# Optimization experiments

Measured on AMD Instinct MI355X. Metric: run time of the kernel, lower is better.

The kernel has to match this reference:

```python
import jax, jax.numpy as jnp
import numpy as np

N = 50000      # nodes
E = 800000     # edges (avg degree 16)
D_IN = 128
D_H = 128
D_OUT = 8


def setup_inputs() -> dict:
    key = jax.random.key(0)
    ks = jax.random.split(key, 12)
    def lin(k, fan_in, shape):
        return (jax.random.normal(k, shape, jnp.float32) / np.float32(np.sqrt(fan_in)))
    return {
        "node_features": jax.random.normal(ks[0], (N, D_IN), jnp.float32),
        "edge_index": jax.random.randint(ks[1], (2, E), 0, N, jnp.int32),
        # 3 GCNConv layers: weight [in, out] + bias [out]
        "W0": lin(ks[2], D_IN, (D_IN, D_H)), "b0": jnp.zeros((D_H,), jnp.float32),
        "W1": lin(ks[3], D_H, (D_H, D_H)),  "b1": jnp.zeros((D_H,), jnp.float32),
        "W2": lin(ks[4], D_H, (D_H, D_H)),  "b2": jnp.zeros((D_H,), jnp.float32),
        # classifier MLP: hidden -> hidden//2 -> output
        "cW1": lin(ks[5], D_H, (D_H, D_H // 2)), "cb1": jnp.zeros((D_H // 2,), jnp.float32),
        "cW2": lin(ks[6], D_H // 2, (D_H // 2, D_OUT)), "cb2": jnp.zeros((D_OUT,), jnp.float32),
    }


def _gcn_norm(edge_index, n):
    # PyG GCNConv default: add self-loops, symmetric D^-1/2 (A+I) D^-1/2 normalization
    loops = jnp.arange(n, dtype=edge_index.dtype)
    src = jnp.concatenate([edge_index[0], loops])   # message sources j
    dst = jnp.concatenate([edge_index[1], loops])   # aggregation targets i
    deg = jax.ops.segment_sum(jnp.ones_like(src, dtype=jnp.float32), dst, num_segments=n)
    dinv = jax.lax.rsqrt(jnp.maximum(deg, 1.0))     # deg >= 1 due to self-loops
    norm = dinv[src] * dinv[dst]                    # [E+N]
    return src, dst, norm


def _gcn_conv(x, W, b, src, dst, norm, n):
    h = x @ W                                        # [N, out] dense transform first (PyG order)
    msg = h[src] * norm[:, None]                     # gather + scale  [E+N, out]
    out = jax.ops.segment_sum(msg, dst, num_segments=n)  # scatter-add
    return out + b


def reference(node_features, edge_index, W0, b0, W1, b1, W2, b2, cW1, cb1, cW2, cb2):
    n = node_features.shape[0]
    src, dst, norm = _gcn_norm(edge_index, n)
    x = jax.nn.relu(_gcn_conv(node_features, W0, b0, src, dst, norm, n))  # dropout is identity in eval
    x = jax.nn.relu(_gcn_conv(x, W1, b1, src, dst, norm, n))
    x = _gcn_conv(x, W2, b2, src, dst, norm, n)       # last conv: no relu/dropout
    # classifier MLP (dropout identity in eval)
    h = jax.nn.relu(x @ cW1 + cb1)
    return h @ cW2 + cb2                              # [N, D_OUT]
```

## Files before the change

### kernel.cpp

```cpp
#include <hip/hip_runtime.h>
#include <hip/hip_fp16.h>


#define CAP 48
#define FPG 256

using half8v  = __attribute__((ext_vector_type(8))) _Float16;
using float4v = __attribute__((ext_vector_type(4))) float;

__global__ __launch_bounds__(256) void fill_kernel(const int* __restrict__ src,
                                                   const int* __restrict__ dst, int e, int n,
                                                   const float* __restrict__ W0,
                                                   const float* __restrict__ W1,
                                                   const float* __restrict__ W2,
                                                   const float* __restrict__ cW1,
                                                   const float* __restrict__ cb1,
                                                   const float* __restrict__ b2,
                                                   int* __restrict__ cnt,
                                                   unsigned short* __restrict__ col,
                                                   __half* __restrict__ Wf0,
                                                   __half* __restrict__ Wf1,
                                                   __half* __restrict__ Wfc,
                                                   float* __restrict__ bc) {
    int b = blockIdx.x;
    int tid = threadIdx.x;
    const int FILLB = 8 * FPG;
    if (b < FILLB) {
        int g = b & 7;
        int cb = b >> 3;
        int npp = (n + 7) >> 3;
        int lo = g * npp;
        int hi = min(lo + npp, n);
        int step = FPG * 256;
        int base = cb * 256 + tid;
        int dv[13], sv[13];
        #pragma unroll
        for (int k = 0; k < 13; k++) {
            int i = base + k * step;
            if (i < e) {
                dv[k] = __builtin_nontemporal_load(dst + i);
                sv[k] = __builtin_nontemporal_load(src + i);
            }
        }
        #pragma unroll
        for (int k = 0; k < 13; k++) {
            int i = base + k * step;
            if (i < e) {
                int d = dv[k];
                if (d >= lo && d < hi) {
                    int c = atomicAdd(&cnt[d], 1);
                    if (c < CAP) col[d * CAP + c] = (unsigned short)sv[k];
                }
            }
        }
        return;
    }
    b -= FILLB;
    if (b < 16) {
        int t = b * 256 + tid;
        const float* W = (t < 2048) ? W0 : W1;
        __half* Wf = (t < 2048) ? Wf0 : Wf1;
        int u = t & 2047;
        int lane = u & 63, tile = (u >> 6) & 7, kk = u >> 9;
        int k0 = kk * 32 + (lane >> 4) * 8;
        int nn = tile * 16 + (lane & 15);
        __half tmp[8];
        #pragma unroll
        for (int j = 0; j < 8; j++) tmp[j] = __float2half(W[(k0 + j) * 128 + nn]);
        *(float4*)(Wf + (size_t)u * 8) = *(const float4*)tmp;
        return;
    }
    b -= 16;
    if (b < 4) {
        int u = b * 256 + tid;
        int lane = u & 63, tile = (u >> 6) & 3, kk = u >> 8;
        int k0 = kk * 32 + (lane >> 4) * 8;
        int nn = tile * 16 + (lane & 15);
        float a[8] = {};
        for (int m = 0; m < 128; m++) {
            float c = cW1[m * 64 + nn];
            #pragma unroll
            for (int j = 0; j < 8; j++) a[j] = fmaf(W2[(k0 + j) * 128 + m], c, a[j]);
        }
        __half tmp[8];
        #pragma unroll
        for (int j = 0; j < 8; j++) tmp[j] = __float2half(a[j]);
        *(float4*)(Wfc + (size_t)u * 8) = *(const float4*)tmp;
        return;
    }
    if (tid < 64) {
        float a = cb1[tid];
        for (int k = 0; k < 128; k++) a = fmaf(b2[k], cW1[k * 64 + tid], a);
        bc[tid] = a;
    }
}

__global__ __launch_bounds__(256) void gemm0_mfma(const float* __restrict__ x,
                                                  const __half* __restrict__ Wf,
                                                  const int* __restrict__ cnt,
                                                  __half* __restrict__ out, int n) {
    int tid = threadIdx.x;
    int wv = tid >> 6, lane = tid & 63;
    int row0 = blockIdx.x * 64 + wv * 16;
    int m = lane & 15, q = lane >> 4;
    int ra = min(row0 + m, n - 1);
    const float* xrow = x + (size_t)ra * 128 + q * 8;
    const _Float16* wf = (const _Float16*)Wf + (size_t)lane * 8;
    float4v acc[8] = {};
    #pragma unroll
    for (int kk = 0; kk < 4; kk++) {
        float4 xa = *(const float4*)(xrow + kk * 32);
        float4 xb = *(const float4*)(xrow + kk * 32 + 4);
        half8v a;
        a[0] = (_Float16)xa.x; a[1] = (_Float16)xa.y;
        a[2] = (_Float16)xa.z; a[3] = (_Float16)xa.w;
        a[4] = (_Float16)xb.x; a[5] = (_Float16)xb.y;
        a[6] = (_Float16)xb.z; a[7] = (_Float16)xb.w;
        #pragma unroll
        for (int t8 = 0; t8 < 8; t8++) {
            half8v bfr = *(const half8v*)(wf + (size_t)(kk * 8 + t8) * 512);
            acc[t8] = __builtin_amdgcn_mfma_f32_16x16x32_f16(a, bfr, acc[t8], 0, 0, 0);
        }
    }
    int rowv[4];
    float dr[4];
    #pragma unroll
    for (int r = 0; r < 4; r++) {
        rowv[r] = row0 + q * 4 + r;
        dr[r] = (rowv[r] < n) ? rsqrtf((float)(cnt[rowv[r]] + 1)) : 0.f;
    }
    #pragma unroll
    for (int t8 = 0; t8 < 8; t8++) {
        #pragma unroll
        for (int r = 0; r < 4; r++) {
            if (rowv[r] < n)
                out[(size_t)(t8 >> 1) * n * 32 + (size_t)rowv[r] * 32 + (t8 & 1) * 16 + m] =
                    __float2half(acc[t8][r] * dr[r]);
        }
    }
}

__global__ __launch_bounds__(256) void gemm_mfma(const __half* __restrict__ x,
                                                 const __half* __restrict__ Wf,
                                                 const int* __restrict__ cnt,
                                                 __half* __restrict__ out, int n) {
    int tid = threadIdx.x;
    int wv = tid >> 6, lane = tid & 63;
    int row0 = blockIdx.x * 64 + wv * 16;
    int m = lane & 15, q = lane >> 4;
    int ra = min(row0 + m, n - 1);
    const _Float16* xb = (const _Float16*)x;
    const _Float16* wf = (const _Float16*)Wf + (size_t)lane * 8;
    float4v acc[8] = {};
    #pragma unroll
    for (int kk = 0; kk < 4; kk++) {
        int tki = kk * 2 + (q >> 1);
        half8v a = *(const half8v*)(xb + (size_t)(tki >> 1) * n * 32 + (size_t)ra * 32 +
                                    (tki & 1) * 16 + (q & 1) * 8);
        #pragma unroll
        for (int t8 = 0; t8 < 8; t8++) {
            half8v bfr = *(const half8v*)(wf + (size_t)(kk * 8 + t8) * 512);
            acc[t8] = __builtin_amdgcn_mfma_f32_16x16x32_f16(a, bfr, acc[t8], 0, 0, 0);
        }
    }
    int rowv[4];
    float dr[4];
    #pragma unroll
    for (int r = 0; r < 4; r++) {
        rowv[r] = row0 + q * 4 + r;
        dr[r] = (rowv[r] < n) ? rsqrtf((float)(cnt[rowv[r]] + 1)) : 0.f;
    }
    #pragma unroll
    for (int t8 = 0; t8 < 8; t8++) {
        #pragma unroll
        for (int r = 0; r < 4; r++) {
            if (rowv[r] < n)
                out[(size_t)(t8 >> 1) * n * 32 + (size_t)rowv[r] * 32 + (t8 & 1) * 16 + m] =
                    __float2half(acc[t8][r] * dr[r]);
        }
    }
}

__global__ __launch_bounds__(256) void agg_tiled(const __half* __restrict__ hin,
                                                 const int* __restrict__ cnt,
                                                 const unsigned short* __restrict__ col,
                                                 const float* __restrict__ bias,
                                                 __half* __restrict__ hout,
                                                 int n, int relu, int scale_out) {
    int ft = blockIdx.x & 3;
    int nb = blockIdx.x >> 2;
    int tid = threadIdx.x;
    int node = nb * 64 + (tid >> 2);
    int q = tid & 3;
    int ic = min(node, n - 1);
    const _Float16* hsl = (const _Float16*)hin + (size_t)ft * n * 32 + q * 8;
    int ci = cnt[ic];
    int len = min(ci, CAP);
    float di = rsqrtf((float)(ci + 1));
    half8v s = *(const half8v*)(hsl + (size_t)ic * 32);
    float acc[8];
    #pragma unroll
    for (int t = 0; t < 8; t++) acc[t] = (float)s[t];
    const unsigned short* crow = col + ic * CAP;
    int nfull = len >> 4;
    for (int f = 0; f < nfull; f++) {
        int k0 = f * 16;
        uint4 ca = *(const uint4*)(crow + k0);
        uint4 cb = *(const uint4*)(crow + k0 + 8);
        int j[16];
        j[0]  = ca.x & 0xffff; j[1]  = ca.x >> 16;
        j[2]  = ca.y & 0xffff; j[3]  = ca.y >> 16;
        j[4]  = ca.z & 0xffff; j[5]  = ca.z >> 16;
        j[6]  = ca.w & 0xffff; j[7]  = ca.w >> 16;
        j[8]  = cb.x & 0xffff; j[9]  = cb.x >> 16;
        j[10] = cb.y & 0xffff; j[11] = cb.y >> 16;
        j[12] = cb.z & 0xffff; j[13] = cb.z >> 16;
        j[14] = cb.w & 0xffff; j[15] = cb.w >> 16;
        half8v v[16];
        #pragma unroll
        for (int u = 0; u < 16; u++) v[u] = *(const half8v*)(hsl + (size_t)j[u] * 32);
        #pragma unroll
        for (int u = 0; u < 16; u++) {
            #pragma unroll
            for (int t = 0; t < 8; t++) acc[t] += (float)v[u][t];
        }
    }
    int k0 = nfull * 16;
    if (k0 < len) {
        int rem = len - k0;
        uint4 ca = *(const uint4*)(crow + k0);
        uint4 cb = *(const uint4*)(crow + k0 + 8);
        int j[16];
        j[0]  = ca.x & 0xffff; j[1]  = ca.x >> 16;
        j[2]  = ca.y & 0xffff; j[3]  = ca.y >> 16;
        j[4]  = ca.z & 0xffff; j[5]  = ca.z >> 16;
        j[6]  = ca.w & 0xffff; j[7]  = ca.w >> 16;
        j[8]  = cb.x & 0xffff; j[9]  = cb.x >> 16;
        j[10] = cb.y & 0xffff; j[11] = cb.y >> 16;
        j[12] = cb.z & 0xffff; j[13] = cb.z >> 16;
        j[14] = cb.w & 0xffff; j[15] = cb.w >> 16;
        float w[16];
        half8v v[16];
        #pragma unroll
        for (int u = 0; u < 16; u++) {
            bool val = u < rem;
            w[u] = val ? 1.f : 0.f;
            int jj = val ? j[u] : ic;
            v[u] = *(const half8v*)(hsl + (size_t)jj * 32);
        }
        #pragma unroll
        for (int u = 0; u < 16; u++) {
            #pragma unroll
            for (int t = 0; t < 8; t++) acc[t] = fmaf(w[u], (float)v[u][t], acc[t]);
        }
    }
    if (node < n) {
        float post = scale_out ? di : 1.f;
        half8v o;
        #pragma unroll
        for (int t = 0; t < 8; t++) {
            float bv = bias ? bias[ft * 32 + q * 8 + t] : 0.f;
            float a = fmaf(acc[t], di, bv);
            if (relu) a = fmaxf(a, 0.f);
            o[t] = (_Float16)(a * post);
        }
        *(half8v*)((_Float16*)hout + (size_t)ft * n * 32 + (size_t)node * 32 + q * 8) = o;
    }
}

__global__ __launch_bounds__(256) void gemmc_cls(const __half* __restrict__ g,
                                                 const __half* __restrict__ Wfc,
                                                 const float* __restrict__ bc,
                                                 const float* __restrict__ cW2,
                                                 const float* __restrict__ cb2,
                                                 float* __restrict__ out, int n) {
    __shared__ float hs[64 * 65];
    int tid = threadIdx.x;
    int wv = tid >> 6, lane = tid & 63;
    int row0 = blockIdx.x * 64 + wv * 16;
    int m = lane & 15, q = lane >> 4;
    int ra = min(row0 + m, n - 1);
    const _Float16* xb = (const _Float16*)g;
    const _Float16* wf = (const _Float16*)Wfc + (size_t)lane * 8;
    float4v acc[4] = {};
    #pragma unroll
    for (int kk = 0; kk < 4; kk++) {
        int tki = kk * 2 + (q >> 1);
        half8v a = *(const half8v*)(xb + (size_t)(tki >> 1) * n * 32 + (size_t)ra * 32 +
                                    (tki & 1) * 16 + (q & 1) * 8);
        #pragma unroll
        for (int t8 = 0; t8 < 4; t8++) {
            half8v bfr = *(const half8v*)(wf + (size_t)(kk * 4 + t8) * 512);
            acc[t8] = __builtin_amdgcn_mfma_f32_16x16x32_f16(a, bfr, acc[t8], 0, 0, 0);
        }
    }
    #pragma unroll
    for (int t8 = 0; t8 < 4; t8++) {
        float bb = bc[t8 * 16 + m];
        #pragma unroll
        for (int r = 0; r < 4; r++) {
            int rl = wv * 16 + q * 4 + r;
            hs[rl * 65 + t8 * 16 + m] = fmaxf(acc[t8][r] + bb, 0.f);
        }
    }
    __syncthreads();
    #pragma unroll
    for (int p = 0; p < 2; p++) {
        int idx = p * 256 + tid;
        int rl = idx >> 3, c2 = idx & 7;
        int row = blockIdx.x * 64 + rl;
        if (row < n) {
            float a = cb2[c2];
            const float* hr = &hs[rl * 65];
            #pragma unroll 8
            for (int k = 0; k < 64; k++) a = fmaf(hr[k], cW2[k * 8 + c2], a);
            out[row * 8 + c2] = a;
        }
    }
}

extern "C" void kernel_launch(void* const* d_in, const int* in_sizes, int n_in,
                              void* d_out, int out_size, void* d_ws, size_t ws_size,
                              hipStream_t stream) {
    const float* x   = (const float*)d_in[0];
    const int*   ei  = (const int*)d_in[1];
    const float* W0  = (const float*)d_in[2];
    const float* b0  = (const float*)d_in[3];
    const float* W1  = (const float*)d_in[4];
    const float* b1  = (const float*)d_in[5];
    const float* W2  = (const float*)d_in[6];
    const float* b2  = (const float*)d_in[7];
    const float* cW1 = (const float*)d_in[8];
    const float* cb1 = (const float*)d_in[9];
    const float* cW2 = (const float*)d_in[10];
    const float* cb2 = (const float*)d_in[11];
    float* out = (float*)d_out;

    int N = in_sizes[0] / 128;
    int E = in_sizes[1] / 2;
    const int* src = ei;
    const int* dst = ei + E;

    char* ws = (char*)d_ws;
    size_t off = 0;
    auto alloc = [&](size_t bytes) {
        void* p = ws + off;
        off = (off + bytes + 255) & ~(size_t)255;
        return p;
    };
    int* cnt              = (int*)alloc((size_t)N * 4);
    unsigned short* col   = (unsigned short*)alloc((size_t)N * CAP * 2);
    __half* Wf0           = (__half*)alloc((size_t)128 * 128 * 2);
    __half* Wf1           = (__half*)alloc((size_t)128 * 128 * 2);
    __half* Wfc           = (__half*)alloc((size_t)128 * 64 * 2);
    float* bc             = (float*)alloc(64 * 4);
    __half* hA            = (__half*)alloc((size_t)N * 128 * 2);
    __half* hB            = (__half*)alloc((size_t)N * 128 * 2);

    hipMemsetAsync(cnt, 0, (size_t)N * 4, stream);

    fill_kernel<<<8 * FPG + 21, 256, 0, stream>>>(src, dst, E, N, W0, W1, W2,
                                                  cW1, cb1, b2,
                                                  cnt, col, Wf0, Wf1, Wfc, bc);

    int NBLK = (N + 63) / 64;
    int ABLK = ((N + 63) / 64) * 4;
    gemm0_mfma<<<NBLK, 256, 0, stream>>>(x, Wf0, cnt, hA, N);
    agg_tiled<<<ABLK, 256, 0, stream>>>(hA, cnt, col, b0, hB, N, 1, 0);
    gemm_mfma<<<NBLK, 256, 0, stream>>>(hB, Wf1, cnt, hA, N);
    agg_tiled<<<ABLK, 256, 0, stream>>>(hA, cnt, col, b1, hB, N, 1, 1);
    agg_tiled<<<ABLK, 256, 0, stream>>>(hB, cnt, col, (const float*)0, hA, N, 0, 0);
    gemmc_cls<<<NBLK, 256, 0, stream>>>(hA, Wfc, bc, cW2, cb2, out, N);
}
```

Baseline: 246.0 us.

## Replace 8-pass edge filter with bucket partition then per-range scatter

Replaces the fill kernel, which read every edge 8 times (once per destination range), with a two-phase build. A partition kernel reads each edge once and appends packed (dst,src) pairs into 8 destination-range buckets, using ballot-aggregated atomics across 8 sub-histogram copies. A scatter kernel then walks each bucket and fills the CSR-like col array, so atomics within a block stay in one node range for locality. This adds an extra kernel launch and an intermediate buffer aliased onto hA. It also relies on a fixed bucket capacity (CAPHG) and on packing dst and src into 16 bits each, which only holds while N stays below 65536.

```diff
diff --git a/kernel.cpp b/kernel.cpp
--- a/kernel.cpp
+++ b/kernel.cpp
@@ -3,96 +3,118 @@
 
 
 #define CAP 48
-#define FPG 256
+#define EPB 1024
+#define CAPHG 16384
+#define SBLK 256
 
 using half8v  = __attribute__((ext_vector_type(8))) _Float16;
 using float4v = __attribute__((ext_vector_type(4))) float;
 
-__global__ __launch_bounds__(256) void fill_kernel(const int* __restrict__ src,
-                                                   const int* __restrict__ dst, int e, int n,
-                                                   const float* __restrict__ W0,
-                                                   const float* __restrict__ W1,
-                                                   const float* __restrict__ W2,
-                                                   const float* __restrict__ cW1,
-                                                   const float* __restrict__ cb1,
-                                                   const float* __restrict__ b2,
-                                                   int* __restrict__ cnt,
-                                                   unsigned short* __restrict__ col,
-                                                   __half* __restrict__ Wf0,
-                                                   __half* __restrict__ Wf1,
-                                                   __half* __restrict__ Wfc,
-                                                   float* __restrict__ bc) {
-    int b = blockIdx.x;
-    int tid = threadIdx.x;
-    const int FILLB = 8 * FPG;
-    if (b < FILLB) {
-        int g = b & 7;
-        int cb = b >> 3;
-        int npp = (n + 7) >> 3;
-        int lo = g * npp;
-        int hi = min(lo + npp, n);
-        int step = FPG * 256;
-        int base = cb * 256 + tid;
-        int dv[13], sv[13];
-        #pragma unroll
-        for (int k = 0; k < 13; k++) {
-            int i = base + k * step;
-            if (i < e) {
-                dv[k] = __builtin_nontemporal_load(dst + i);
-                sv[k] = __builtin_nontemporal_load(src + i);
-            }
-        }
-        #pragma unroll
-        for (int k = 0; k < 13; k++) {
-            int i = base + k * step;
-            if (i < e) {
-                int d = dv[k];
-                if (d >= lo && d < hi) {
-                    int c = atomicAdd(&cnt[d], 1);
-                    if (c < CAP) col[d * CAP + c] = (unsigned short)sv[k];
-                }
-            }
-        }
-        return;
-    }
-    b -= FILLB;
-    if (b < 16) {
-        int t = b * 256 + tid;
-        const float* W = (t < 2048) ? W0 : W1;
-        __half* Wf = (t < 2048) ? Wf0 : Wf1;
-        int u = t & 2047;
-        int lane = u & 63, tile = (u >> 6) & 7, kk = u >> 9;
-        int k0 = kk * 32 + (lane >> 4) * 8;
-        int nn = tile * 16 + (lane & 15);
-        __half tmp[8];
-        #pragma unroll
-        for (int j = 0; j < 8; j++) tmp[j] = __float2half(W[(k0 + j) * 128 + nn]);
-        *(float4*)(Wf + (size_t)u * 8) = *(const float4*)tmp;
-        return;
-    }
-    b -= 16;
-    if (b < 4) {
-        int u = b * 256 + tid;
-        int lane = u & 63, tile = (u >> 6) & 3, kk = u >> 8;
-        int k0 = kk * 32 + (lane >> 4) * 8;
-        int nn = tile * 16 + (lane & 15);
-        float a[8] = {};
-        for (int m = 0; m < 128; m++) {
-            float c = cW1[m * 64 + nn];
-            #pragma unroll
-            for (int j = 0; j < 8; j++) a[j] = fmaf(W2[(k0 + j) * 128 + m], c, a[j]);
-        }
-        __half tmp[8];
-        #pragma unroll
-        for (int j = 0; j < 8; j++) tmp[j] = __float2half(a[j]);
-        *(float4*)(Wfc + (size_t)u * 8) = *(const float4*)tmp;
-        return;
-    }
-    if (tid < 64) {
-        float a = cb1[tid];
-        for (int k = 0; k < 128; k++) a = fmaf(b2[k], cW1[k * 64 + tid], a);
-        bc[tid] = a;
-    }
+__global__ __launch_bounds__(256) void partition_kernel(
+    const int* __restrict__ src, const int* __restrict__ dst, int e,
+    float bscale, int pb,
+    const float* __restrict__ W0, const float* __restrict__ W1,
+    const float* __restrict__ W2, const float* __restrict__ cW1,
+    const float* __restrict__ cb1, const float* __restrict__ b2,
+    unsigned int* __restrict__ bcnt, unsigned int* __restrict__ buf,
+    __half* __restrict__ Wf0, __half* __restrict__ Wf1,
+    __half* __restrict__ Wfc, float* __restrict__ bc) {
+  int b = blockIdx.x;
+  int tid = threadIdx.x;
+  if (b < pb) {
+    int h = b & 7;
+    unsigned int* hcnt = bcnt + h * 8;
+    unsigned int* hbuf = buf + (size_t)h * 8 * CAPHG;
+    int base = b * EPB + tid;
+    int lane = tid & 63;
+    #pragma unroll
+    for (int k = 0; k < 4; k++) {
+      int i = base + k * 256;
+      bool valid = i < e;
+      int d = 0, s = 0;
+      if (valid) {
+        d = __builtin_nontemporal_load(dst + i);
+        s = __builtin_nontemporal_load(src + i);
+      }
+      int g = valid ? min(7, (int)((float)d * bscale)) : -1;
+      unsigned int pk = ((unsigned int)d << 16) | (unsigned int)(s & 0xffff);
+      for (int bb = 0; bb < 8; bb++) {
+        unsigned long long m = __ballot(g == bb);
+        if (m == 0) continue;
+        int leader = __ffsll((long long)m) - 1;
+        unsigned int c64 = (unsigned int)__popcll(m);
+        unsigned int pos = 0;
+        if (lane == leader) pos = atomicAdd(&hcnt[bb], c64);
+        pos = __shfl(pos, leader);
+        if (g == bb) {
+          unsigned int idx = pos + (unsigned int)__popcll(m & ((1ull << lane) - 1));
+          if (idx < CAPHG) hbuf[(size_t)bb * CAPHG + idx] = pk;
+        }
+      }
+    }
+    return;
+  }
+  b -= pb;
+  if (b < 16) {
+    int t = b * 256 + tid;
+    const float* W = (t < 2048) ? W0 : W1;
+    __half* Wf = (t < 2048) ? Wf0 : Wf1;
+    int u = t & 2047;
+    int lane = u & 63, tile = (u >> 6) & 7, kk = u >> 9;
+    int k0 = kk * 32 + (lane >> 4) * 8;
+    int nn = tile * 16 + (lane & 15);
+    __half tmp[8];
+    #pragma unroll
+    for (int j = 0; j < 8; j++) tmp[j] = __float2half(W[(k0 + j) * 128 + nn]);
+    *(float4*)(Wf + (size_t)u * 8) = *(const float4*)tmp;
+    return;
+  }
+  b -= 16;
+  if (b < 4) {
+    int u = b * 256 + tid;
+    int lane = u & 63, tile = (u >> 6) & 3, kk = u >> 8;
+    int k0 = kk * 32 + (lane >> 4) * 8;
+    int nn = tile * 16 + (lane & 15);
+    float a[8] = {};
+    for (int m = 0; m < 128; m++) {
+      float c = cW1[m * 64 + nn];
+      #pragma unroll
+      for (int j = 0; j < 8; j++) a[j] = fmaf(W2[(k0 + j) * 128 + m], c, a[j]);
+    }
+    __half tmp[8];
+    #pragma unroll
+    for (int j = 0; j < 8; j++) tmp[j] = __float2half(a[j]);
+    *(float4*)(Wfc + (size_t)u * 8) = *(const float4*)tmp;
+    return;
+  }
+  if (tid < 64) {
+    float a = cb1[tid];
+    for (int k = 0; k < 128; k++) a = fmaf(b2[k], cW1[k * 64 + tid], a);
+    bc[tid] = a;
+  }
+}
+
+__global__ __launch_bounds__(256) void scatter_kernel(
+    const unsigned int* __restrict__ bcnt, const unsigned int* __restrict__ buf,
+    int* __restrict__ cnt, unsigned short* __restrict__ col) {
+  int g = blockIdx.x & 7;
+  int sb = blockIdx.x >> 3;
+  int tid = threadIdx.x;
+  unsigned int start = (unsigned int)sb * 256 + tid;
+  #pragma unroll
+  for (int t = 0; t < (8 * CAPHG) / (SBLK * 256); t++) {
+    unsigned int j = start + (unsigned int)t * (SBLK * 256);
+    unsigned int h = j >> 14;
+    unsigned int i = j & (CAPHG - 1);
+    unsigned int nb = min(bcnt[h * 8 + g], (unsigned int)CAPHG);
+    if (i < nb) {
+      unsigned int pk = buf[(((size_t)h * 8 + g) << 14) + i];
+      int d = (int)(pk >> 16);
+      int s = (int)(pk & 0xffff);
+      int c = atomicAdd(&cnt[d], 1);
+      if (c < CAP) col[d * CAP + c] = (unsigned short)s;
+    }
+  }
 }
 
 __global__ __launch_bounds__(256) void gemm0_mfma(const float* __restrict__ x,
@@ -349,6 +371,7 @@
         return p;
     };
     int* cnt              = (int*)alloc((size_t)N * 4);
+    unsigned int* bcnt    = (unsigned int*)alloc(256);
     unsigned short* col   = (unsigned short*)alloc((size_t)N * CAP * 2);
     __half* Wf0           = (__half*)alloc((size_t)128 * 128 * 2);
     __half* Wf1           = (__half*)alloc((size_t)128 * 128 * 2);
@@ -356,12 +379,17 @@
     float* bc             = (float*)alloc(64 * 4);
     __half* hA            = (__half*)alloc((size_t)N * 128 * 2);
     __half* hB            = (__half*)alloc((size_t)N * 128 * 2);
-
-    hipMemsetAsync(cnt, 0, (size_t)N * 4, stream);
-
-    fill_kernel<<<8 * FPG + 21, 256, 0, stream>>>(src, dst, E, N, W0, W1, W2,
-                                                  cW1, cb1, b2,
-                                                  cnt, col, Wf0, Wf1, Wfc, bc);
+    unsigned int* buf     = (unsigned int*)hA;
+
+    hipMemsetAsync(cnt, 0, (((size_t)N * 4 + 255) & ~(size_t)255) + 256, stream);
+
+    int PB = ((((E + EPB - 1) / EPB) + 7) / 8) * 8;
+    float bscale = 8.0f / (float)N;
+
+    partition_kernel<<<PB + 21, 256, 0, stream>>>(src, dst, E, bscale, PB,
+                                                  W0, W1, W2, cW1, cb1, b2,
+                                                  bcnt, buf, Wf0, Wf1, Wfc, bc);
+    scatter_kernel<<<8 * SBLK, 256, 0, stream>>>(bcnt, buf, cnt, col);
 
     int NBLK = (N + 63) / 64;
     int ABLK = ((N + 63) / 64) * 4;
```

After: 718.7 us. 192% more time.

## Apply fused classifier weight before last aggregation to halve gather width

Applied to the files above, without the earlier changes.

The last GCN layer's weight W2 is already folded into cW1 (Wfc, bias bc). This change applies that 128→64 projection before the final neighbour aggregation instead of after it, since aggregation is linear, so the last gather-and-scatter moves 64 features per node instead of 128. The bias and ReLU are then applied inside the aggregation, and a light classifier kernel does only the 64→8 product. This adds a small GEMM kernel and an extra fp16 rounding point before aggregation, which may shift accuracy slightly.

```diff
diff --git a/kernel.cpp b/kernel.cpp
--- a/kernel.cpp
+++ b/kernel.cpp
@@ -181,14 +181,50 @@
     }
 }
 
+__global__ __launch_bounds__(256) void gemm_t_mfma(const __half* __restrict__ x,
+                                                   const __half* __restrict__ Wf,
+                                                   __half* __restrict__ out, int n) {
+    int tid = threadIdx.x;
+    int wv = tid >> 6, lane = tid & 63;
+    int row0 = blockIdx.x * 64 + wv * 16;
+    int m = lane & 15, q = lane >> 4;
+    int ra = min(row0 + m, n - 1);
+    const _Float16* xb = (const _Float16*)x;
+    const _Float16* wf = (const _Float16*)Wf + (size_t)lane * 8;
+    float4v acc[4] = {};
+    #pragma unroll
+    for (int kk = 0; kk < 4; kk++) {
+        int tki = kk * 2 + (q >> 1);
+        half8v a = *(const half8v*)(xb + (size_t)(tki >> 1) * n * 32 + (size_t)ra * 32 +
+                                    (tki & 1) * 16 + (q & 1) * 8);
+        #pragma unroll
+        for (int t8 = 0; t8 < 4; t8++) {
+            half8v bfr = *(const half8v*)(wf + (size_t)(kk * 4 + t8) * 512);
+            acc[t8] = __builtin_amdgcn_mfma_f32_16x16x32_f16(a, bfr, acc[t8], 0, 0, 0);
+        }
+    }
+    int rowv[4];
+    #pragma unroll
+    for (int r = 0; r < 4; r++) rowv[r] = row0 + q * 4 + r;
+    #pragma unroll
+    for (int t8 = 0; t8 < 4; t8++) {
+        #pragma unroll
+        for (int r = 0; r < 4; r++) {
+            if (rowv[r] < n)
+                out[(size_t)(t8 >> 1) * n * 32 + (size_t)rowv[r] * 32 + (t8 & 1) * 16 + m] =
+                    __float2half(acc[t8][r]);
+        }
+    }
+}
+
 __global__ __launch_bounds__(256) void agg_tiled(const __half* __restrict__ hin,
                                                  const int* __restrict__ cnt,
                                                  const unsigned short* __restrict__ col,
                                                  const float* __restrict__ bias,
                                                  __half* __restrict__ hout,
-                                                 int n, int relu, int scale_out) {
-    int ft = blockIdx.x & 3;
-    int nb = blockIdx.x >> 2;
+                                                 int n, int relu, int scale_out, int ftsh) {
+    int ft = blockIdx.x & ((1 << ftsh) - 1);
+    int nb = blockIdx.x >> ftsh;
     int tid = threadIdx.x;
     int node = nb * 64 + (tid >> 2);
     int q = tid & 3;
@@ -268,52 +304,31 @@
     }
 }
 
-__global__ __launch_bounds__(256) void gemmc_cls(const __half* __restrict__ g,
-                                                 const __half* __restrict__ Wfc,
-                                                 const float* __restrict__ bc,
-                                                 const float* __restrict__ cW2,
-                                                 const float* __restrict__ cb2,
-                                                 float* __restrict__ out, int n) {
-    __shared__ float hs[64 * 65];
-    int tid = threadIdx.x;
-    int wv = tid >> 6, lane = tid & 63;
-    int row0 = blockIdx.x * 64 + wv * 16;
-    int m = lane & 15, q = lane >> 4;
-    int ra = min(row0 + m, n - 1);
-    const _Float16* xb = (const _Float16*)g;
-    const _Float16* wf = (const _Float16*)Wfc + (size_t)lane * 8;
-    float4v acc[4] = {};
-    #pragma unroll
-    for (int kk = 0; kk < 4; kk++) {
-        int tki = kk * 2 + (q >> 1);
-        half8v a = *(const half8v*)(xb + (size_t)(tki >> 1) * n * 32 + (size_t)ra * 32 +
-                                    (tki & 1) * 16 + (q & 1) * 8);
-        #pragma unroll
-        for (int t8 = 0; t8 < 4; t8++) {
-            half8v bfr = *(const half8v*)(wf + (size_t)(kk * 4 + t8) * 512);
-            acc[t8] = __builtin_amdgcn_mfma_f32_16x16x32_f16(a, bfr, acc[t8], 0, 0, 0);
-        }
-    }
-    #pragma unroll
-    for (int t8 = 0; t8 < 4; t8++) {
-        float bb = bc[t8 * 16 + m];
-        #pragma unroll
-        for (int r = 0; r < 4; r++) {
-            int rl = wv * 16 + q * 4 + r;
-            hs[rl * 65 + t8 * 16 + m] = fmaxf(acc[t8][r] + bb, 0.f);
-        }
+__global__ __launch_bounds__(256) void cls_kernel(const __half* __restrict__ h,
+                                                  const float* __restrict__ cW2,
+                                                  const float* __restrict__ cb2,
+                                                  float* __restrict__ out, int n) {
+    __shared__ _Float16 hs[64][72];
+    int tid = threadIdx.x;
+    int node0 = blockIdx.x * 64;
+    int nl = tid >> 2, q = tid & 3;
+    int ic = min(node0 + nl, n - 1);
+    #pragma unroll
+    for (int ft = 0; ft < 2; ft++) {
+        half8v v = *(const half8v*)((const _Float16*)h + (size_t)ft * n * 32 +
+                                    (size_t)ic * 32 + q * 8);
+        *(half8v*)&hs[nl][ft * 32 + q * 8] = v;
     }
     __syncthreads();
     #pragma unroll
     for (int p = 0; p < 2; p++) {
         int idx = p * 256 + tid;
         int rl = idx >> 3, c2 = idx & 7;
-        int row = blockIdx.x * 64 + rl;
+        int row = node0 + rl;
         if (row < n) {
             float a = cb2[c2];
-            const float* hr = &hs[rl * 65];
             #pragma unroll 8
-            for (int k = 0; k < 64; k++) a = fmaf(hr[k], cW2[k * 8 + c2], a);
+            for (int k = 0; k < 64; k++) a = fmaf((float)hs[rl][k], cW2[k * 8 + c2], a);
             out[row * 8 + c2] = a;
         }
     }
@@ -364,11 +379,11 @@
                                                   cnt, col, Wf0, Wf1, Wfc, bc);
 
     int NBLK = (N + 63) / 64;
-    int ABLK = ((N + 63) / 64) * 4;
     gemm0_mfma<<<NBLK, 256, 0, stream>>>(x, Wf0, cnt, hA, N);
-    agg_tiled<<<ABLK, 256, 0, stream>>>(hA, cnt, col, b0, hB, N, 1, 0);
+    agg_tiled<<<NBLK * 4, 256, 0, stream>>>(hA, cnt, col, b0, hB, N, 1, 0, 2);
     gemm_mfma<<<NBLK, 256, 0, stream>>>(hB, Wf1, cnt, hA, N);
-    agg_tiled<<<ABLK, 256, 0, stream>>>(hA, cnt, col, b1, hB, N, 1, 1);
-    agg_tiled<<<ABLK, 256, 0, stream>>>(hB, cnt, col, (const float*)0, hA, N, 0, 0);
-    gemmc_cls<<<NBLK, 256, 0, stream>>>(hA, Wfc, bc, cW2, cb2, out, N);
-}
+    agg_tiled<<<NBLK * 4, 256, 0, stream>>>(hA, cnt, col, b1, hB, N, 1, 1, 2);
+    gemm_t_mfma<<<NBLK, 256, 0, stream>>>(hB, Wfc, hA, N);
+    agg_tiled<<<NBLK * 2, 256, 0, stream>>>(hA, cnt, col, bc, hB, N, 1, 0, 1);
+    cls_kernel<<<NBLK, 256, 0, stream>>>(hB, cW2, cb2, out, N);
+}
```

After: 247.2 us. No clear change (+0.5%).
